# Performance work log

Hardware: AMD Instinct MI355X
Metric: run time of the kernel (lower is better)

Reference implementation:

```python
import jax, jax.numpy as jnp
import numpy as np

D_MODEL = 1024
NUM_HEADS = 16
ROPE_THETA = 10000.0


def setup_inputs() -> dict:
    key = jax.random.key(0)
    ks = jax.random.split(key, 5)
    B, S, D = 4, 2048, D_MODEL
    scale = 1.0 / np.sqrt(D)
    return {
        "x": jax.random.normal(ks[0], (B, S, D), dtype=jnp.float32),
        "Wq": jax.random.normal(ks[1], (D, D), dtype=jnp.float32) * scale,
        "Wk": jax.random.normal(ks[2], (D, D), dtype=jnp.float32) * scale,
        "Wv": jax.random.normal(ks[3], (D, D), dtype=jnp.float32) * scale,
        "Wo": jax.random.normal(ks[4], (D, D), dtype=jnp.float32) * scale,
        "token_positions": jnp.arange(S, dtype=jnp.int32),
    }


def _rope(x, pos, theta=ROPE_THETA):
    # x: (b, h, s, d); interleaved-pair rotary embedding
    d = x.shape[-1]
    inv_freq = 1.0 / (theta ** (jnp.arange(0, d, 2, dtype=jnp.float32) / d))  # (d/2,)
    ang = pos.astype(jnp.float32)[:, None] * inv_freq[None, :]  # (s, d/2)
    cos, sin = jnp.cos(ang), jnp.sin(ang)
    x1, x2 = x[..., ::2], x[..., 1::2]
    out = jnp.stack([x1 * cos - x2 * sin, x1 * sin + x2 * cos], axis=-1)
    return out.reshape(x.shape)


def reference(x, Wq, Wk, Wv, Wo, token_positions):
    B, S, D = x.shape
    H = NUM_HEADS
    dh = D // H
    # torch nn.Linear(bias=False): y = x @ W.T
    q = jnp.einsum('bsd,ed->bse', x, Wq).reshape(B, S, H, dh).transpose(0, 2, 1, 3)
    k = jnp.einsum('bsd,ed->bse', x, Wk).reshape(B, S, H, dh).transpose(0, 2, 1, 3)
    v = jnp.einsum('bsd,ed->bse', x, Wv).reshape(B, S, H, dh).transpose(0, 2, 1, 3)
    q = _rope(q, token_positions)
    k = _rope(k, token_positions)
    scores = jnp.einsum('bhqd,bhkd->bhqk', q, k) / jnp.sqrt(jnp.array(dh, x.dtype))
    causal = jnp.tril(jnp.ones((S, S), dtype=bool))
    scores = jnp.where(causal, scores, jnp.array(-jnp.inf, scores.dtype))
    probs = jax.nn.softmax(scores, axis=-1)
    attn = jnp.einsum('bhqk,bhkd->bhqd', probs, v)  # (b, h, s, dh)
    attn = attn.transpose(0, 2, 1, 3).reshape(B, S, D)
    return jnp.einsum('bsd,ed->bse', attn, Wo)
```

## Files before the change

### kernel.cpp

```cpp
#include <hip/hip_runtime.h>
#include <hip/hip_bf16.h>
#include <stdint.h>

#define S_LEN 2048
#define BATCH 4
#define NH    16
#define DH    64
#define DM    1024
#define MTOT  (BATCH*S_LEN)

typedef short bf16x8 __attribute__((ext_vector_type(8)));
typedef float f32x4 __attribute__((ext_vector_type(4)));
typedef uint32_t u32x4 __attribute__((ext_vector_type(4)));

__device__ __forceinline__ uint16_t f2bf(float f) {
  union { float f; uint32_t i; } c; c.f = f;
  uint32_t r = c.i + 0x7fffu + ((c.i >> 16) & 1u);
  return (uint16_t)(r >> 16);
}
__device__ __forceinline__ float bf2f(uint16_t u) {
  union { uint32_t i; float f; } c; c.i = ((uint32_t)u) << 16; return c.f;
}

__device__ __forceinline__ uint32_t cvt_pk_bf16(float a, float b) {
  uint32_t r;
  asm("v_cvt_pk_bf16_f32 %0, %1, %2" : "=v"(r) : "v"(a), "v"(b));
  return r;
}

__device__ __forceinline__ void async_copy16(void* lds, const void* g) {
  __builtin_amdgcn_global_load_lds(
      (const __attribute__((address_space(1))) void*)g,
      (__attribute__((address_space(3))) void*)lds, 16, 0, 0);
}

__global__ __launch_bounds__(256) void cvt_f32_bf16(const float* __restrict__ in,
                                                    uint16_t* __restrict__ out, int n4) {
  int stride = gridDim.x * blockDim.x;
  for (int i = blockIdx.x * blockDim.x + threadIdx.x; i < n4; i += stride) {
    float4 v = ((const float4*)in)[i];
    ushort4 o;
    o.x = f2bf(v.x); o.y = f2bf(v.y); o.z = f2bf(v.z); o.w = f2bf(v.w);
    ((ushort4*)out)[i] = o;
  }
}

__global__ __launch_bounds__(256) void cvt_w4(const float* __restrict__ wq,
                                              const float* __restrict__ wk,
                                              const float* __restrict__ wv,
                                              const float* __restrict__ wo,
                                              uint16_t* __restrict__ out) {
  const int sel = blockIdx.y;
  const float* src = sel == 0 ? wq : sel == 1 ? wk : sel == 2 ? wv : wo;
  uint16_t* dst = out + (size_t)sel * DM * DM;
  const int n4 = DM * DM / 4;
  const int stride = gridDim.x * blockDim.x;
  for (int i = blockIdx.x * blockDim.x + threadIdx.x; i < n4; i += stride) {
    float4 v = ((const float4*)src)[i];
    ushort4 o;
    o.x = f2bf(v.x); o.y = f2bf(v.y); o.z = f2bf(v.z); o.w = f2bf(v.w);
    ((ushort4*)dst)[i] = o;
  }
}

template<int MODE, int BN>
__global__ __launch_bounds__(256) void gemm_bt(const uint16_t* __restrict__ A,
                                               const uint16_t* __restrict__ Bw,
                                               void* __restrict__ outp,
                                               const int* __restrict__ pos) {
  constexpr int K = DM;
  constexpr int NT = K / 32;
  constexpr int WC = BN / 2;
  constexpr int NF = WC / 16;
  __shared__ __align__(16) uint16_t lA[3][128 * 32];
  __shared__ __align__(16) uint16_t lB[3][BN * 32];
  const int tid = threadIdx.x;
  const int w = tid >> 6, lane = tid & 63;
  const int l15 = lane & 15, lhi = lane >> 4;
  const int wr = w >> 1, wc = w & 1;

  const int nx = gridDim.x, nwg = nx * gridDim.y;
  const int flat = blockIdx.y * nx + blockIdx.x;
  const int wg = (flat & 7) * (nwg >> 3) + (flat >> 3);
  const int bm = (wg / nx) * 128, bn = (wg % nx) * BN;

  const int srow = tid >> 2;
  const int cb = (tid & 3) * 16;

  auto stage = [&](int b, int t) {
    const int k0 = t * 32;
#pragma unroll
    for (int i = 0; i < 2; ++i)
      async_copy16((char*)lA[b] + i * 4096 + w * 1024,
                   (const char*)A + ((size_t)(bm + i * 64 + srow) * K + k0) * 2 + cb);
#pragma unroll
    for (int i = 0; i < BN / 64; ++i)
      async_copy16((char*)lB[b] + i * 4096 + w * 1024,
                   (const char*)Bw + ((size_t)(bn + i * 64 + srow) * K + k0) * 2 + cb);
  };

  f32x4 acc[4][NF] = {};

  stage(0, 0);
  stage(1, 1);
  if constexpr (BN == 128) asm volatile("s_waitcnt vmcnt(4)" ::: "memory");
  else                     asm volatile("s_waitcnt vmcnt(3)" ::: "memory");
  __builtin_amdgcn_s_barrier();
  __builtin_amdgcn_sched_barrier(0);

  int cur = 0;
  for (int t = 0; t < NT; ++t) {
    const bool pre = (t + 2 < NT);
    int bnext = cur + 2; if (bnext >= 3) bnext -= 3;
    if (pre) stage(bnext, t + 2);

    bf16x8 af[4], bfr[NF];
#pragma unroll
    for (int mf = 0; mf < 4; ++mf)
      af[mf] = *(const bf16x8*)((const char*)lA[cur] +
                                (wr * 64 + mf * 16 + l15) * 64 + lhi * 16);
#pragma unroll
    for (int nf = 0; nf < NF; ++nf)
      bfr[nf] = *(const bf16x8*)((const char*)lB[cur] +
                                 (wc * WC + nf * 16 + l15) * 64 + lhi * 16);
    __builtin_amdgcn_s_setprio(1);
#pragma unroll
    for (int mf = 0; mf < 4; ++mf)
#pragma unroll
      for (int nf = 0; nf < NF; ++nf)
        acc[mf][nf] = __builtin_amdgcn_mfma_f32_16x16x32_bf16(af[mf], bfr[nf], acc[mf][nf], 0, 0, 0);
    __builtin_amdgcn_s_setprio(0);

    if (pre) {
      if constexpr (BN == 128) asm volatile("s_waitcnt vmcnt(4)" ::: "memory");
      else                     asm volatile("s_waitcnt vmcnt(3)" ::: "memory");
    } else {
      asm volatile("s_waitcnt vmcnt(0)" ::: "memory");
    }
    __builtin_amdgcn_s_barrier();
    __builtin_amdgcn_sched_barrier(0);
    cur = cur + 1 == 3 ? 0 : cur + 1;
  }

  if (MODE == 0) {
    const int tsel = bn >> 10;
    uint16_t* out = (uint16_t*)outp + (size_t)tsel * ((size_t)MTOT * DM);
    if (tsel < 2) {
      const float l2t_32 = 0.41524101186092074f;
      const float qsc = tsel == 0 ? 0.18033688011112042f : 1.0f;
#pragma unroll
      for (int mf = 0; mf < 4; ++mf) {
        float ps[4];
#pragma unroll
        for (int r = 0; r < 4; ++r) {
          const int m = bm + wr * 64 + mf * 16 + lhi * 4 + r;
          ps[r] = (float)pos[m & (S_LEN - 1)];
        }
#pragma unroll
        for (int nf = 0; nf < NF; ++nf) {
          const int n = bn + wc * WC + nf * 16 + l15;
          const int e = n & 1023;
          const int h = e >> 6, d = e & 63;
          const float inv = __builtin_amdgcn_exp2f(-(float)(d >> 1) * l2t_32);
#pragma unroll
          for (int r = 0; r < 4; ++r) {
            const int m = bm + wr * 64 + mf * 16 + lhi * 4 + r;
            const int b = m >> 11, s = m & (S_LEN - 1);
            const float v = acc[mf][nf][r];
            const float p = __shfl_xor(v, 1);
            const float ang = ps[r] * inv;
            const float cs = __cosf(ang) * qsc, sn = __sinf(ang) * qsc;
            const float val = (l15 & 1) ? (p * sn + v * cs) : (v * cs - p * sn);
            out[(((size_t)(b * NH + h) * S_LEN + s) << 6) + d] = f2bf(val);
          }
        }
      }
    } else {
#pragma unroll
      for (int mf = 0; mf < 4; ++mf)
#pragma unroll
        for (int nf = 0; nf < NF; ++nf)
#pragma unroll
          for (int r = 0; r < 4; ++r) {
            const int m = bm + wr * 64 + mf * 16 + lhi * 4 + r;
            const int n = bn + wc * WC + nf * 16 + l15;
            const int b = m >> 11, s = m & (S_LEN - 1);
            const int e = n & 1023;
            const int h = e >> 6, d = e & 63;
            out[(((size_t)(b * NH + h) * S_LEN + s) << 6) + d] = f2bf(acc[mf][nf][r]);
          }
    }
  } else {
    float* out = (float*)outp;
#pragma unroll
    for (int mf = 0; mf < 4; ++mf)
#pragma unroll
      for (int nf = 0; nf < NF; ++nf)
#pragma unroll
        for (int r = 0; r < 4; ++r) {
          const int m = bm + wr * 64 + mf * 16 + lhi * 4 + r;
          const int n = bn + wc * WC + nf * 16 + l15;
          out[(size_t)m * DM + n] = acc[mf][nf][r];
        }
  }
}

__global__ __launch_bounds__(256) void transpose_v(const uint16_t* __restrict__ v,
                                                   uint16_t* __restrict__ vt) {
  __shared__ uint16_t t[64 * 65];
  const int bh = blockIdx.y, s0 = blockIdx.x * 64;
  const uint16_t* vb = v + (size_t)bh * S_LEN * 64 + (size_t)s0 * 64;
  uint16_t* ob = vt + (size_t)bh * 64 * S_LEN + s0;
  for (int o = threadIdx.x; o < 64 * 64; o += 256) {
    const int r = o >> 6, c = o & 63;
    t[c * 65 + r] = vb[(size_t)r * 64 + c];
  }
  __syncthreads();
  for (int o = threadIdx.x; o < 64 * 64; o += 256) {
    const int d = o >> 6, p = o & 63;
    const int sp = (p & 32) | (((p >> 2) & 3) << 3) | (((p >> 4) & 1) << 2) | (p & 3);
    ob[(size_t)d * S_LEN + sp] = t[d * 65 + p];
  }
}

__global__ __launch_bounds__(512, 2) void attn_kernel(const uint16_t* __restrict__ q,
                                                      const uint16_t* __restrict__ kk,
                                                      const uint16_t* __restrict__ vt,
                                                      uint16_t* __restrict__ o) {
  const int bh = blockIdx.y;
  const int p = blockIdx.x;
  const int jA = 15 - p, jB = p;
  const int tid = threadIdx.x;
  const int w = __builtin_amdgcn_readfirstlane(tid >> 6);
  const int lane = tid & 63;
  const int l15 = lane & 15, lhi = lane >> 4;
  const uint16_t* qb = q + (size_t)bh * S_LEN * DH;
  const uint16_t* kb = kk + (size_t)bh * S_LEN * DH;
  const uint16_t* vb = vt + (size_t)bh * DH * S_LEN;

  __shared__ uint16_t lK[2][128 * 64];
  __shared__ uint16_t lV[2][64 * 128];

  const int krow_l = lane >> 3;
  const int scK = (lane & 7) ^ krow_l;
  const int vrow_l = lane >> 4;

  auto stage = [&](int b, int t) {
    const int k0 = t * 128;
#pragma unroll
    for (int i = 0; i < 2; ++i) {
      const int krow = w * 16 + i * 8 + krow_l;
      async_copy16((char*)lK[b] + w * 2048 + i * 1024 + lane * 16,
                   (const char*)kb + ((size_t)(k0 + krow) * 64 + scK * 8) * 2);
      const int vd = w * 8 + i * 4 + vrow_l;
      const int scV = (lane & 15) ^ (vd & 15);
      async_copy16((char*)lV[b] + w * 2048 + i * 1024 + lane * 16,
                   (const char*)vb + ((size_t)vd * S_LEN + k0 + scV * 8) * 2);
    }
  };

  stage(0, 0);
  asm volatile("s_waitcnt vmcnt(0)" ::: "memory");
  __syncthreads();

  int cur = 0;
  const int b_out = bh >> 4, h_out = bh & 15;

  bf16x8 qf[2][2];
#pragma unroll
  for (int fr = 0; fr < 2; ++fr) {
    const int q0 = (fr ? jB : jA) * 128 + w * 16;
#pragma unroll
    for (int c = 0; c < 2; ++c)
      qf[fr][c] = *(const bf16x8*)(qb + (size_t)(q0 + l15) * DH + c * 32 + lhi * 8);
  }

  f32x4 oa[2][4] = {};
  float mr[2] = {-1e30f, -1e30f}, lr[2] = {0.f, 0.f};

  const int nt = jA + 1;
  for (int t = 0; t < nt; ++t) {
    if (t + 1 < nt) stage(cur ^ 1, t + 1);

#pragma unroll
    for (int fr = 0; fr < 2; ++fr) {
      if (fr == 1 && t > jB) continue;
      const int jq = fr ? jB : jA;
      const bool diag = (t == jq);
      const int fMf = diag ? w : 7;
      const int fE  = diag ? (w | 1) : 7;
      const int cE  = diag ? (w >> 1) : 3;

      f32x4 sf[8];
      __builtin_amdgcn_s_setprio(1);
#pragma unroll
      for (int f = 0; f < 8; ++f) {
        f32x4 z = {0.f, 0.f, 0.f, 0.f};
        if (f <= fMf) {
          const int kr = f * 16 + l15;
          const char* kbase = (const char*)lK[cur] + kr * 128;
          bf16x8 kf0 = *(const bf16x8*)(kbase + ((lhi ^ (kr & 7)) << 4));
          bf16x8 kf1 = *(const bf16x8*)(kbase + (((4 + lhi) ^ (kr & 7)) << 4));
          z = __builtin_amdgcn_mfma_f32_16x16x32_bf16(kf0, qf[fr][0], z, 0, 0, 0);
          z = __builtin_amdgcn_mfma_f32_16x16x32_bf16(kf1, qf[fr][1], z, 0, 0, 0);
        }
        sf[f] = z;
      }
      __builtin_amdgcn_s_setprio(0);

      if (diag) {
        const int qrow = w * 16 + l15;
#pragma unroll
        for (int f = 0; f < 8; ++f)
          if (f <= fE)
#pragma unroll
            for (int r = 0; r < 4; ++r) {
              const int kv = f * 16 + lhi * 4 + r;
              if (kv > qrow) sf[f][r] = -1e30f;
            }
      }

      float pm = -1e30f;
#pragma unroll
      for (int f = 0; f < 8; ++f)
        if (f <= fE)
#pragma unroll
          for (int r = 0; r < 4; ++r) pm = fmaxf(pm, sf[f][r]);
      pm = fmaxf(pm, __shfl_xor(pm, 16));
      pm = fmaxf(pm, __shfl_xor(pm, 32));

      if (!__all(pm <= mr[fr] + 8.0f)) {
        const float mn = fmaxf(mr[fr], pm);
        const float resc = __builtin_amdgcn_exp2f(mr[fr] - mn);
        mr[fr] = mn;
        lr[fr] *= resc;
#pragma unroll
        for (int r = 0; r < 4; ++r) {
          const float rb = __shfl(resc, (lhi << 2) + r);
#pragma unroll
          for (int df = 0; df < 4; ++df) oa[fr][df][r] *= rb;
        }
      }

      float rs = 0.f;
#pragma unroll
      for (int f = 0; f < 8; ++f)
        if (f <= fE)
#pragma unroll
          for (int r = 0; r < 4; ++r) {
            const float pv = __builtin_amdgcn_exp2f(sf[f][r] - mr[fr]);
            sf[f][r] = pv;
            rs += pv;
          }
      rs += __shfl_xor(rs, 16);
      rs += __shfl_xor(rs, 32);
      lr[fr] += rs;

#pragma unroll
      for (int c = 0; c < 4; ++c) {
        if (c <= cE) {
          u32x4 u;
          u.x = cvt_pk_bf16(sf[2 * c][0], sf[2 * c][1]);
          u.y = cvt_pk_bf16(sf[2 * c][2], sf[2 * c][3]);
          u.z = cvt_pk_bf16(sf[2 * c + 1][0], sf[2 * c + 1][1]);
          u.w = cvt_pk_bf16(sf[2 * c + 1][2], sf[2 * c + 1][3]);
          bf16x8 pa = __builtin_bit_cast(bf16x8, u);
          __builtin_amdgcn_s_setprio(1);
#pragma unroll
          for (int df = 0; df < 4; ++df) {
            const int vr = df * 16 + l15;
            bf16x8 vf = *(const bf16x8*)((const char*)lV[cur] + vr * 256 +
                                         ((((c << 2) + lhi) ^ (vr & 15)) << 4));
            oa[fr][df] = __builtin_amdgcn_mfma_f32_16x16x32_bf16(pa, vf, oa[fr][df], 0, 0, 0);
          }
          __builtin_amdgcn_s_setprio(0);
        }
      }
    }

    asm volatile("s_waitcnt vmcnt(0)" ::: "memory");
    __syncthreads();
    cur ^= 1;
  }

#pragma unroll
  for (int fr = 0; fr < 2; ++fr) {
    const int q0 = (fr ? jB : jA) * 128 + w * 16;
    float inv[4];
#pragma unroll
    for (int r = 0; r < 4; ++r)
      inv[r] = __builtin_amdgcn_rcpf(__shfl(lr[fr], (lhi << 2) + r));
#pragma unroll
    for (int df = 0; df < 4; ++df)
#pragma unroll
      for (int r = 0; r < 4; ++r) {
        const int srow_o = q0 + lhi * 4 + r;
        const float val = oa[fr][df][r] * inv[r];
        const int d = df * 16 + l15;
        o[((size_t)(b_out * S_LEN + srow_o)) * DM + h_out * 64 + d] = f2bf(val);
      }
  }
}

extern "C" void kernel_launch(void* const* d_in, const int* in_sizes, int n_in,
                              void* d_out, int out_size, void* d_ws, size_t ws_size,
                              hipStream_t stream) {
  const float* x = (const float*)d_in[0];
  const float* Wq = (const float*)d_in[1];
  const float* Wk = (const float*)d_in[2];
  const float* Wv = (const float*)d_in[3];
  const float* Wo = (const float*)d_in[4];
  const int* pos = (const int*)d_in[5];

  char* ws = (char*)d_ws;
  size_t off = 0;
  auto alloc = [&](size_t bytes) {
    void* p = ws + off;
    off += (bytes + 255) & ~(size_t)255;
    return p;
  };
  uint16_t* xb    = (uint16_t*)alloc((size_t)MTOT * DM * 2);
  uint16_t* wqkvb = (uint16_t*)alloc((size_t)4 * DM * DM * 2);
  uint16_t* qkvb  = (uint16_t*)alloc((size_t)3 * MTOT * DM * 2);
  uint16_t* vtb   = (uint16_t*)alloc((size_t)MTOT * DM * 2);
  uint16_t* wob = wqkvb + (size_t)3 * DM * DM;
  uint16_t* qb = qkvb;
  uint16_t* kbuf = qkvb + (size_t)MTOT * DM;
  uint16_t* vbuf = qkvb + (size_t)2 * MTOT * DM;
  uint16_t* attnb = xb;

  cvt_f32_bf16<<<2048, 256, 0, stream>>>(x, xb, MTOT * DM / 4);
  cvt_w4<<<dim3(128, 4), 256, 0, stream>>>(Wq, Wk, Wv, Wo, wqkvb);

  gemm_bt<0, 128><<<dim3(24, MTOT / 128), 256, 0, stream>>>(xb, wqkvb, qkvb, pos);

  transpose_v<<<dim3(32, 64), 256, 0, stream>>>(vbuf, vtb);

  attn_kernel<<<dim3(8, 64), 512, 0, stream>>>(qb, kbuf, vtb, attnb);

  gemm_bt<1, 64><<<dim3(16, MTOT / 128), 256, 0, stream>>>(attnb, wob, d_out, nullptr);
}
```

Baseline: 175.8 us.

## Fuse V transpose into QKV GEMM epilogue and merge conversion kernels

```diff
diff --git a/kernel.cpp b/kernel.cpp
--- a/kernel.cpp
+++ b/kernel.cpp
@@ -18,9 +18,6 @@
   uint32_t r = c.i + 0x7fffu + ((c.i >> 16) & 1u);
   return (uint16_t)(r >> 16);
 }
-__device__ __forceinline__ float bf2f(uint16_t u) {
-  union { uint32_t i; float f; } c; c.i = ((uint32_t)u) << 16; return c.f;
-}
 
 __device__ __forceinline__ uint32_t cvt_pk_bf16(float a, float b) {
   uint32_t r;
@@ -34,28 +31,27 @@
       (__attribute__((address_space(3))) void*)lds, 16, 0, 0);
 }
 
-__global__ __launch_bounds__(256) void cvt_f32_bf16(const float* __restrict__ in,
-                                                    uint16_t* __restrict__ out, int n4) {
-  int stride = gridDim.x * blockDim.x;
-  for (int i = blockIdx.x * blockDim.x + threadIdx.x; i < n4; i += stride) {
-    float4 v = ((const float4*)in)[i];
-    ushort4 o;
-    o.x = f2bf(v.x); o.y = f2bf(v.y); o.z = f2bf(v.z); o.w = f2bf(v.w);
-    ((ushort4*)out)[i] = o;
-  }
-}
-
-__global__ __launch_bounds__(256) void cvt_w4(const float* __restrict__ wq,
-                                              const float* __restrict__ wk,
-                                              const float* __restrict__ wv,
-                                              const float* __restrict__ wo,
-                                              uint16_t* __restrict__ out) {
-  const int sel = blockIdx.y;
-  const float* src = sel == 0 ? wq : sel == 1 ? wk : sel == 2 ? wv : wo;
-  uint16_t* dst = out + (size_t)sel * DM * DM;
-  const int n4 = DM * DM / 4;
-  const int stride = gridDim.x * blockDim.x;
-  for (int i = blockIdx.x * blockDim.x + threadIdx.x; i < n4; i += stride) {
+__global__ __launch_bounds__(256) void cvt_all(const float* __restrict__ x,
+                                               const float* __restrict__ wq,
+                                               const float* __restrict__ wk,
+                                               const float* __restrict__ wv,
+                                               const float* __restrict__ wo,
+                                               uint16_t* __restrict__ xb,
+                                               uint16_t* __restrict__ wb) {
+  const int blk = blockIdx.x;
+  const float* src;
+  uint16_t* dst;
+  int n4, b0, nb;
+  if (blk < 512) {
+    src = x; dst = xb; n4 = MTOT * DM / 4; b0 = blk; nb = 512;
+  } else {
+    const int sel = (blk - 512) >> 6;
+    src = sel == 0 ? wq : sel == 1 ? wk : sel == 2 ? wv : wo;
+    dst = wb + (size_t)sel * DM * DM;
+    n4 = DM * DM / 4; b0 = (blk - 512) & 63; nb = 64;
+  }
+  const int stride = nb * 256;
+  for (int i = b0 * 256 + threadIdx.x; i < n4; i += stride) {
     float4 v = ((const float4*)src)[i];
     ushort4 o;
     o.x = f2bf(v.x); o.y = f2bf(v.y); o.z = f2bf(v.z); o.w = f2bf(v.w);
@@ -67,13 +63,17 @@
 __global__ __launch_bounds__(256) void gemm_bt(const uint16_t* __restrict__ A,
                                                const uint16_t* __restrict__ Bw,
                                                void* __restrict__ outp,
+                                               uint16_t* __restrict__ vtp,
                                                const int* __restrict__ pos) {
   constexpr int K = DM;
   constexpr int NT = K / 32;
   constexpr int WC = BN / 2;
   constexpr int NF = WC / 16;
-  __shared__ __align__(16) uint16_t lA[3][128 * 32];
-  __shared__ __align__(16) uint16_t lB[3][BN * 32];
+  constexpr int ASZ = 3 * 128 * 32;
+  constexpr int BSZ = 3 * BN * 32;
+  __shared__ __align__(16) uint16_t sh[ASZ + BSZ];
+  uint16_t* lA = sh;
+  uint16_t* lB = sh + ASZ;
   const int tid = threadIdx.x;
   const int w = tid >> 6, lane = tid & 63;
   const int l15 = lane & 15, lhi = lane >> 4;
@@ -91,11 +91,11 @@
     const int k0 = t * 32;
 #pragma unroll
     for (int i = 0; i < 2; ++i)
-      async_copy16((char*)lA[b] + i * 4096 + w * 1024,
+      async_copy16((char*)(lA + b * 128 * 32) + i * 4096 + w * 1024,
                    (const char*)A + ((size_t)(bm + i * 64 + srow) * K + k0) * 2 + cb);
 #pragma unroll
     for (int i = 0; i < BN / 64; ++i)
-      async_copy16((char*)lB[b] + i * 4096 + w * 1024,
+      async_copy16((char*)(lB + b * BN * 32) + i * 4096 + w * 1024,
                    (const char*)Bw + ((size_t)(bn + i * 64 + srow) * K + k0) * 2 + cb);
   };
 
@@ -117,11 +117,11 @@
     bf16x8 af[4], bfr[NF];
 #pragma unroll
     for (int mf = 0; mf < 4; ++mf)
-      af[mf] = *(const bf16x8*)((const char*)lA[cur] +
+      af[mf] = *(const bf16x8*)((const char*)(lA + cur * 128 * 32) +
                                 (wr * 64 + mf * 16 + l15) * 64 + lhi * 16);
 #pragma unroll
     for (int nf = 0; nf < NF; ++nf)
-      bfr[nf] = *(const bf16x8*)((const char*)lB[cur] +
+      bfr[nf] = *(const bf16x8*)((const char*)(lB + cur * BN * 32) +
                                  (wc * WC + nf * 16 + l15) * 64 + lhi * 16);
     __builtin_amdgcn_s_setprio(1);
 #pragma unroll
@@ -144,8 +144,8 @@
 
   if (MODE == 0) {
     const int tsel = bn >> 10;
-    uint16_t* out = (uint16_t*)outp + (size_t)tsel * ((size_t)MTOT * DM);
     if (tsel < 2) {
+      uint16_t* out = (uint16_t*)outp + (size_t)tsel * ((size_t)MTOT * DM);
       const float l2t_32 = 0.41524101186092074f;
       const float qsc = tsel == 0 ? 0.18033688011112042f : 1.0f;
 #pragma unroll
@@ -176,19 +176,37 @@
         }
       }
     } else {
+      uint16_t* T = sh;
 #pragma unroll
       for (int mf = 0; mf < 4; ++mf)
 #pragma unroll
-        for (int nf = 0; nf < NF; ++nf)
-#pragma unroll
-          for (int r = 0; r < 4; ++r) {
-            const int m = bm + wr * 64 + mf * 16 + lhi * 4 + r;
-            const int n = bn + wc * WC + nf * 16 + l15;
-            const int b = m >> 11, s = m & (S_LEN - 1);
-            const int e = n & 1023;
-            const int h = e >> 6, d = e & 63;
-            out[(((size_t)(b * NH + h) * S_LEN + s) << 6) + d] = f2bf(acc[mf][nf][r]);
-          }
+        for (int nf = 0; nf < NF; ++nf) {
+          const int n = wc * WC + nf * 16 + l15;
+          const int m0 = wr * 64 + mf * 16 + lhi * 4;
+          uint32_t lo = cvt_pk_bf16(acc[mf][nf][0], acc[mf][nf][1]);
+          uint32_t hi = cvt_pk_bf16(acc[mf][nf][2], acc[mf][nf][3]);
+          *(uint2*)(T + n * 136 + m0) = make_uint2(lo, hi);
+        }
+      __syncthreads();
+      const int b = bm >> 11, s0 = bm & (S_LEN - 1);
+      const int ebase = bn & 1023;
+      for (int idx = tid; idx < 2048; idx += 256) {
+        const int n = idx >> 4;
+        const int j0 = (idx & 15) * 8;
+        const int oa_ = j0 & 63;
+        const int pa_ = (j0 & 64) | (oa_ & 0x23) | ((oa_ & 4) << 2) |
+                        ((oa_ & 16) >> 1) | ((oa_ & 8) >> 1);
+        const int ob_ = (j0 + 4) & 63;
+        const int pb_ = (j0 & 64) | (ob_ & 0x23) | ((ob_ & 4) << 2) |
+                        ((ob_ & 16) >> 1) | ((ob_ & 8) >> 1);
+        const uint2 va = *(const uint2*)(T + n * 136 + pa_);
+        const uint2 vb2 = *(const uint2*)(T + n * 136 + pb_);
+        const int e = ebase + n;
+        const int hg = e >> 6, d = e & 63;
+        uint16_t* dst = vtp + ((size_t)(b * NH + hg) * DH + d) * S_LEN + s0 + j0;
+        uint4 o4; o4.x = va.x; o4.y = va.y; o4.z = vb2.x; o4.w = vb2.y;
+        *(uint4*)dst = o4;
+      }
     }
   } else {
     float* out = (float*)outp;
@@ -202,24 +220,6 @@
           const int n = bn + wc * WC + nf * 16 + l15;
           out[(size_t)m * DM + n] = acc[mf][nf][r];
         }
-  }
-}
-
-__global__ __launch_bounds__(256) void transpose_v(const uint16_t* __restrict__ v,
-                                                   uint16_t* __restrict__ vt) {
-  __shared__ uint16_t t[64 * 65];
-  const int bh = blockIdx.y, s0 = blockIdx.x * 64;
-  const uint16_t* vb = v + (size_t)bh * S_LEN * 64 + (size_t)s0 * 64;
-  uint16_t* ob = vt + (size_t)bh * 64 * S_LEN + s0;
-  for (int o = threadIdx.x; o < 64 * 64; o += 256) {
-    const int r = o >> 6, c = o & 63;
-    t[c * 65 + r] = vb[(size_t)r * 64 + c];
-  }
-  __syncthreads();
-  for (int o = threadIdx.x; o < 64 * 64; o += 256) {
-    const int d = o >> 6, p = o & 63;
-    const int sp = (p & 32) | (((p >> 2) & 3) << 3) | (((p >> 4) & 1) << 2) | (p & 3);
-    ob[(size_t)d * S_LEN + sp] = t[d * 65 + p];
   }
 }
 
@@ -421,22 +421,18 @@
   };
   uint16_t* xb    = (uint16_t*)alloc((size_t)MTOT * DM * 2);
   uint16_t* wqkvb = (uint16_t*)alloc((size_t)4 * DM * DM * 2);
-  uint16_t* qkvb  = (uint16_t*)alloc((size_t)3 * MTOT * DM * 2);
+  uint16_t* qkb   = (uint16_t*)alloc((size_t)2 * MTOT * DM * 2);
   uint16_t* vtb   = (uint16_t*)alloc((size_t)MTOT * DM * 2);
   uint16_t* wob = wqkvb + (size_t)3 * DM * DM;
-  uint16_t* qb = qkvb;
-  uint16_t* kbuf = qkvb + (size_t)MTOT * DM;
-  uint16_t* vbuf = qkvb + (size_t)2 * MTOT * DM;
+  uint16_t* qb = qkb;
+  uint16_t* kbuf = qkb + (size_t)MTOT * DM;
   uint16_t* attnb = xb;
 
-  cvt_f32_bf16<<<2048, 256, 0, stream>>>(x, xb, MTOT * DM / 4);
-  cvt_w4<<<dim3(128, 4), 256, 0, stream>>>(Wq, Wk, Wv, Wo, wqkvb);
-
-  gemm_bt<0, 128><<<dim3(24, MTOT / 128), 256, 0, stream>>>(xb, wqkvb, qkvb, pos);
-
-  transpose_v<<<dim3(32, 64), 256, 0, stream>>>(vbuf, vtb);
+  cvt_all<<<768, 256, 0, stream>>>(x, Wq, Wk, Wv, Wo, xb, wqkvb);
+
+  gemm_bt<0, 128><<<dim3(24, MTOT / 128), 256, 0, stream>>>(xb, wqkvb, qkb, vtb, pos);
 
   attn_kernel<<<dim3(8, 64), 512, 0, stream>>>(qb, kbuf, vtb, attnb);
 
-  gemm_bt<1, 64><<<dim3(16, MTOT / 128), 256, 0, stream>>>(attnb, wob, d_out, nullptr);
-}
+  gemm_bt<1, 64><<<dim3(16, MTOT / 128), 256, 0, stream>>>(attnb, wob, d_out, nullptr, nullptr);
+}
```

Result: faster. 167.9 us, median of 3 (-4.5%).
